# Performance work log

Hardware: AMD Instinct MI355X
Metric: run time of the kernel (lower is better)

The kernel has to match this reference:

```python
import jax, jax.numpy as jnp
import numpy as np

B = 1024          # graphs (games)
NPG = 12          # nodes per hand (to_dense_batch max_num_nodes=12)
N = B * NPG       # nodes per node type
EPG = 72          # edges per graph per edge type
E = B * EPG
CARD = 32         # card embedding dim
HID = 256         # hidden_dim
H = 4             # attention heads
L = 3             # num_layers
FIN = 128         # final_dim
LRELU_SLOPE = float(FIN)  # faithful to nn.LeakyReLU(final_dim) bug


def _make_edges(key):
    k1, k2 = jax.random.split(key)
    g = jnp.repeat(jnp.arange(B, dtype=jnp.int32), EPG)
    src = g * NPG + jax.random.randint(k1, (E,), 0, NPG, dtype=jnp.int32)
    dst = g * NPG + jax.random.randint(k2, (E,), 0, NPG, dtype=jnp.int32)
    return jnp.stack([src, dst])


def setup_inputs() -> dict:
    key = jax.random.key(0)
    ks = jax.random.split(key, 24)
    def nrm(k, shape, fan):
        return jax.random.normal(k, shape, jnp.float32) / np.float32(np.sqrt(fan))
    inp = {
        'x_my': jax.random.normal(ks[0], (N, CARD), jnp.float32),
        'x_opp': jax.random.normal(ks[1], (N, CARD), jnp.float32),
        'edge_beats': _make_edges(ks[2]),
        'edge_loses': _make_edges(ks[3]),
        'edge_rev_beats': _make_edges(ks[4]),
        'edge_rev_loses': _make_edges(ks[5]),
        'batch_my': jnp.repeat(jnp.arange(B, dtype=jnp.int32), NPG),
        # input encoder
        'enc_W': nrm(ks[6], (CARD, HID), CARD), 'enc_b': jnp.zeros((HID,), jnp.float32),
        # GATv2 params, axis1 indexes {0: beats(my->opp), 1: rev_loses_to(opp->my)}
        'gat_Wl': nrm(ks[7], (L, 2, HID, H * HID), HID),
        'gat_bl': jnp.zeros((L, 2, H * HID), jnp.float32),
        'gat_Wr': nrm(ks[8], (L, 2, HID, H * HID), HID),
        'gat_br': jnp.zeros((L, 2, H * HID), jnp.float32),
        'gat_att': nrm(ks[9], (L, 2, H, HID), HID),
        'gat_bias': jnp.zeros((L, 2, HID), jnp.float32),
        # CGConv params, axis1 indexes {0: loses_to(my->opp), 1: rev_beats(opp->my)}
        'cg_Wf': nrm(ks[10], (L, 2, 2 * HID, HID), 2 * HID),
        'cg_bf': jnp.zeros((L, 2, HID), jnp.float32),
        'cg_Ws': nrm(ks[11], (L, 2, 2 * HID, HID), 2 * HID),
        'cg_bs': jnp.zeros((L, 2, HID), jnp.float32),
        # nodewise linear per layer
        'node_W': nrm(ks[12], (L, HID, HID), HID),
        'node_b': jnp.zeros((L, HID), jnp.float32),
        # final encoder
        'fin_W1': nrm(ks[13], (HID, FIN), HID), 'fin_b1': jnp.zeros((FIN,), jnp.float32),
        'fin_W2': nrm(ks[14], (FIN, 1), FIN), 'fin_b2': jnp.zeros((1,), jnp.float32),
    }
    return inp


def _gatv2(x_src, x_dst, edge, Wl, bl, Wr, br, att, bias):
    # PyG GATv2Conv, concat=False, add_self_loops=False, negative_slope=0.2
    Nd = x_dst.shape[0]
    xl = (x_src @ Wl + bl).reshape(-1, H, HID)   # [Ns,H,C]
    xr = (x_dst @ Wr + br).reshape(-1, H, HID)   # [Nd,H,C]
    src, dst = edge[0], edge[1]
    e = jax.nn.leaky_relu(xl[src] + xr[dst], 0.2)            # [E,H,C]
    alpha = jnp.einsum('ehc,hc->eh', e, att)                 # [E,H]
    m = jax.ops.segment_max(alpha, dst, num_segments=Nd)     # softmax by dst
    a = jnp.exp(alpha - m[dst])
    denom = jax.ops.segment_sum(a, dst, num_segments=Nd)
    a = a / (denom[dst] + 1e-16)
    out = jax.ops.segment_sum(a[:, :, None] * xl[src], dst, num_segments=Nd)
    return out.mean(axis=1) + bias                           # mean over heads


def _cgconv(x_src, x_dst, edge, Wf, bf, Ws, bs):
    # PyG CGConv: z = [x_i(dst), x_j(src)]; sigmoid gate * softplus; sum; residual
    src, dst = edge[0], edge[1]
    z = jnp.concatenate([x_dst[dst], x_src[src]], axis=-1)   # [E,2*HID]
    msg = jax.nn.sigmoid(z @ Wf + bf) * jax.nn.softplus(z @ Ws + bs)
    return x_dst + jax.ops.segment_sum(msg, dst, num_segments=x_dst.shape[0])


def reference(x_my, x_opp, edge_beats, edge_loses, edge_rev_beats, edge_rev_loses,
              batch_my, enc_W, enc_b, gat_Wl, gat_bl, gat_Wr, gat_br, gat_att,
              gat_bias, cg_Wf, cg_bf, cg_Ws, cg_bs, node_W, node_b,
              fin_W1, fin_b1, fin_W2, fin_b2):
    h_my = x_my @ enc_W + enc_b
    h_opp = x_opp @ enc_W + enc_b
    for l in range(L):
        # destination opponent_hand: GAT(beats) + CG(loses_to)  (HeteroConv aggr='sum')
        opp_new = _gatv2(h_my, h_opp, edge_beats, gat_Wl[l, 0], gat_bl[l, 0],
                         gat_Wr[l, 0], gat_br[l, 0], gat_att[l, 0], gat_bias[l, 0]) \
                + _cgconv(h_my, h_opp, edge_loses, cg_Wf[l, 0], cg_bf[l, 0],
                          cg_Ws[l, 0], cg_bs[l, 0])
        # destination my_hand: CG(rev_beats) + GAT(rev_loses_to)
        my_new = _cgconv(h_opp, h_my, edge_rev_beats, cg_Wf[l, 1], cg_bf[l, 1],
                         cg_Ws[l, 1], cg_bs[l, 1]) \
               + _gatv2(h_opp, h_my, edge_rev_loses, gat_Wl[l, 1], gat_bl[l, 1],
                        gat_Wr[l, 1], gat_br[l, 1], gat_att[l, 1], gat_bias[l, 1])
        h_my = my_new @ node_W[l] + node_b[l]
        h_opp = opp_new @ node_W[l] + node_b[l]
    f = jax.nn.leaky_relu(h_my @ fin_W1 + fin_b1, LRELU_SLOPE)
    logits = f @ fin_W2 + fin_b2                              # [N,1]
    # to_dense_batch with exactly NPG sorted nodes per graph == reshape
    return logits.reshape(B, NPG)
```

## Files before the change

### kernel.cpp

```cpp
#include <hip/hip_runtime.h>

#define NNODES 12288
#define ETOT   73728
#define NGR    1024
#define LOG2E  1.442695041f
#define LN2    0.6931471806f

typedef __attribute__((ext_vector_type(8))) short short8;
typedef __attribute__((ext_vector_type(4))) float f32x4;

__device__ __forceinline__ unsigned short f2b(float f) {
  return __builtin_bit_cast(unsigned short, (__bf16)f);
}
__device__ __forceinline__ float b2f(unsigned short u) {
  return __uint_as_float(((unsigned)u) << 16);
}
__device__ __forceinline__ void load_lds16(const void* g, void* l) {
  __builtin_amdgcn_global_load_lds(
      (const __attribute__((address_space(1))) unsigned int*)g,
      (__attribute__((address_space(3))) unsigned int*)l, 16, 0, 0);
}
__device__ __forceinline__ unsigned fenc(float f) {
  unsigned u = __float_as_uint(f);
  return (u & 0x80000000u) ? ~u : (u | 0x80000000u);
}
__device__ __forceinline__ float fdec(unsigned e) {
  unsigned u = (e & 0x80000000u) ? (e & 0x7FFFFFFFu) : ~e;
  return __uint_as_float(u);
}

__device__ __forceinline__ const unsigned short* pnode(
    const unsigned short* P, int col0, int node) {
  return P + ((size_t)(col0 >> 7) * NNODES + node) * 128 + (col0 & 127);
}

__global__ void pack_kernel(
    const float* __restrict__ gat_Wl, const float* __restrict__ gat_Wr,
    const float* __restrict__ cg_Wf, const float* __restrict__ cg_Ws,
    const float* __restrict__ node_W, const float* __restrict__ enc_W,
    const float* __restrict__ fin_W1,
    const float* __restrict__ gat_bl, const float* __restrict__ gat_br,
    const float* __restrict__ cg_bf, const float* __restrict__ cg_bs,
    const float* __restrict__ x_my, const float* __restrict__ x_opp,
    unsigned short* __restrict__ wt_my, unsigned short* __restrict__ wt_opp,
    unsigned short* __restrict__ node_wt, unsigned short* __restrict__ enc_wt,
    unsigned short* __restrict__ fin_w1t,
    float* __restrict__ bias_my, float* __restrict__ bias_opp,
    unsigned short* __restrict__ xb)
{
  int idx = blockIdx.x * 256 + threadIdx.x;
  if (idx < 2 * 2359296) {
    int which = idx >= 2359296;
    int t = which ? idx - 2359296 : idx;
    int l = t / 786432;
    int r = t - l * 786432;
    int j = r & 7, lane = (r >> 3) & 63, blk = r >> 9;
    int kb = blk & 7, nb = blk >> 3;
    int n = nb * 16 + (lane & 15);
    int k = kb * 32 + (lane >> 4) * 8 + j;
    float v;
    if (!which) {
      if (n < 1024)      v = gat_Wl[((l*2+0)*256 + k)*1024 + n];
      else if (n < 2048) v = gat_Wr[((l*2+1)*256 + k)*1024 + (n-1024)];
      else if (n < 2304) v = cg_Wf[((l*2+0)*512 + 256 + k)*256 + (n-2048)];
      else if (n < 2560) v = cg_Ws[((l*2+0)*512 + 256 + k)*256 + (n-2304)];
      else if (n < 2816) v = cg_Wf[((l*2+1)*512 + k)*256 + (n-2560)];
      else               v = cg_Ws[((l*2+1)*512 + k)*256 + (n-2816)];
      wt_my[t] = f2b(v);
    } else {
      if (n < 1024)      v = gat_Wr[((l*2+0)*256 + k)*1024 + n];
      else if (n < 2048) v = gat_Wl[((l*2+1)*256 + k)*1024 + (n-1024)];
      else if (n < 2304) v = cg_Wf[((l*2+0)*512 + k)*256 + (n-2048)];
      else if (n < 2560) v = cg_Ws[((l*2+0)*512 + k)*256 + (n-2304)];
      else if (n < 2816) v = cg_Wf[((l*2+1)*512 + 256 + k)*256 + (n-2560)];
      else               v = cg_Ws[((l*2+1)*512 + 256 + k)*256 + (n-2816)];
      wt_opp[t] = f2b(v);
    }
    return;
  }
  idx -= 2 * 2359296;
  if (idx < 196608) {
    int l = idx / 65536, r = idx - l * 65536;
    int j = r & 7, lane = (r >> 3) & 63, blk = r >> 9;
    int kb = blk & 7, nb = blk >> 3;
    int n = nb * 16 + (lane & 15);
    int k = kb * 32 + (lane >> 4) * 8 + j;
    node_wt[idx] = f2b(node_W[(l*256 + k)*256 + n]);
    return;
  }
  idx -= 196608;
  if (idx < 8192) {
    int r = idx;
    int j = r & 7, lane = (r >> 3) & 63, blk = r >> 9;
    int nb = blk;
    int n = nb * 16 + (lane & 15);
    int k = (lane >> 4) * 8 + j;
    enc_wt[idx] = f2b(enc_W[k*256 + n]);
    return;
  }
  idx -= 8192;
  if (idx < 32768) {
    int r = idx;
    int j = r & 7, lane = (r >> 3) & 63, blk = r >> 9;
    int kb = blk & 7, nb = blk >> 3;
    int n = nb * 16 + (lane & 15);
    int k = kb * 32 + (lane >> 4) * 8 + j;
    fin_w1t[idx] = f2b(fin_W1[k*128 + n]);
    return;
  }
  idx -= 32768;
  if (idx < 9216) {
    int l = idx / 3072, n = idx - l * 3072;
    float v;
    if (n < 1024)      v = gat_bl[(l*2+0)*1024 + n];
    else if (n < 2048) v = gat_br[(l*2+1)*1024 + (n-1024)];
    else if (n < 2560) v = 0.f;
    else if (n < 2816) v = cg_bf[(l*2+1)*256 + (n-2560)];
    else               v = cg_bs[(l*2+1)*256 + (n-2816)];
    bias_my[idx] = v;
    return;
  }
  idx -= 9216;
  if (idx < 9216) {
    int l = idx / 3072, n = idx - l * 3072;
    float v;
    if (n < 1024)      v = gat_br[(l*2+0)*1024 + n];
    else if (n < 2048) v = gat_bl[(l*2+1)*1024 + (n-1024)];
    else if (n < 2304) v = cg_bf[(l*2+0)*256 + (n-2048)];
    else if (n < 2560) v = cg_bs[(l*2+0)*256 + (n-2304)];
    else               v = 0.f;
    bias_opp[idx] = v;
    return;
  }
  idx -= 9216;
  if (idx < 2 * 393216) {
    xb[idx] = f2b(idx < 393216 ? x_my[idx] : x_opp[idx - 393216]);
  }
}

__global__ __launch_bounds__(256) void gemm64(
    const unsigned short* __restrict__ A, const unsigned short* __restrict__ Ab,
    int lda,
    const unsigned short* __restrict__ Wp, const unsigned short* __restrict__ Wpb,
    const float* __restrict__ bias, const float* __restrict__ biasb,
    unsigned short* __restrict__ C, unsigned short* __restrict__ Cb,
    int ldc, int K, int act, int bx_split, int colblk)
{
  __shared__ __align__(16) unsigned short lA[64 * 256];
  const int tid = threadIdx.x;
  const int lane = tid & 63;
  const int w = tid >> 6;
  const int wr = w >> 1, wc = w & 1;
  const int r0 = lane & 15, kq = lane >> 4;
  const int KT = K >> 5;
  const int gm = (K >> 3) - 1;
  const int rmask = gm > 7 ? 7 : gm;
  const int gsh = __popc((unsigned)gm);

  const unsigned short *Ap, *Wsel;
  const float* bp;
  unsigned short* Cp;
  int tileM;
  if ((int)blockIdx.x < bx_split) {
    Ap = A;  Wsel = Wp;  bp = bias;  Cp = C;  tileM = blockIdx.x * 64;
  } else {
    Ap = Ab; Wsel = Wpb; bp = biasb; Cp = Cb; tileM = (blockIdx.x - bx_split) * 64;
  }
  const int tileN = blockIdx.y * 128;

  for (int rd = 0; rd < KT; ++rd) {
    int idx = rd * 256 + tid;
    int row = idx >> gsh;
    int g = idx & gm;
    load_lds16(Ap + (size_t)(tileM + row) * lda + ((g ^ (row & rmask)) << 3),
               (char*)lA + idx * 16);
  }

  const int nblk0 = (tileN >> 4) + wc * 4;
  const unsigned short* wn0 = Wsel + ((size_t)(nblk0 + 0) * KT * 64 + lane) * 8;
  const unsigned short* wn1 = Wsel + ((size_t)(nblk0 + 1) * KT * 64 + lane) * 8;
  const unsigned short* wn2 = Wsel + ((size_t)(nblk0 + 2) * KT * 64 + lane) * 8;
  const unsigned short* wn3 = Wsel + ((size_t)(nblk0 + 3) * KT * 64 + lane) * 8;

  short8 b0_0 = *(const short8*)wn0;
  short8 b0_1 = *(const short8*)wn1;
  short8 b0_2 = *(const short8*)wn2;
  short8 b0_3 = *(const short8*)wn3;
  short8 b1_0 = b0_0, b1_1 = b0_1, b1_2 = b0_2, b1_3 = b0_3;
  if (KT > 1) {
    b1_0 = *(const short8*)(wn0 + 512);
    b1_1 = *(const short8*)(wn1 + 512);
    b1_2 = *(const short8*)(wn2 + 512);
    b1_3 = *(const short8*)(wn3 + 512);
  }

  f32x4 acc[2][4];
#pragma unroll
  for (int m = 0; m < 2; ++m)
#pragma unroll
    for (int n = 0; n < 4; ++n)
      acc[m][n] = (f32x4){0.f, 0.f, 0.f, 0.f};

  const int rb0 = (wr * 32 + r0) * K;
  const int rb1 = (wr * 32 + 16 + r0) * K;
  const int rx = r0 & rmask;

  __syncthreads();

  for (int kt = 0; kt < KT; ++kt) {
    short8 b2_0 = b1_0, b2_1 = b1_1, b2_2 = b1_2, b2_3 = b1_3;
    if (kt + 2 < KT) {
      const int o = (kt + 2) * 512;
      b2_0 = *(const short8*)(wn0 + o);
      b2_1 = *(const short8*)(wn1 + o);
      b2_2 = *(const short8*)(wn2 + o);
      b2_3 = *(const short8*)(wn3 + o);
    }
    const int p = (((kt << 2) + kq) ^ rx) * 8;
    short8 af0 = *(const short8*)&lA[rb0 + p];
    short8 af1 = *(const short8*)&lA[rb1 + p];
    acc[0][0] = __builtin_amdgcn_mfma_f32_16x16x32_bf16(b0_0, af0, acc[0][0], 0, 0, 0);
    acc[0][1] = __builtin_amdgcn_mfma_f32_16x16x32_bf16(b0_1, af0, acc[0][1], 0, 0, 0);
    acc[0][2] = __builtin_amdgcn_mfma_f32_16x16x32_bf16(b0_2, af0, acc[0][2], 0, 0, 0);
    acc[0][3] = __builtin_amdgcn_mfma_f32_16x16x32_bf16(b0_3, af0, acc[0][3], 0, 0, 0);
    acc[1][0] = __builtin_amdgcn_mfma_f32_16x16x32_bf16(b0_0, af1, acc[1][0], 0, 0, 0);
    acc[1][1] = __builtin_amdgcn_mfma_f32_16x16x32_bf16(b0_1, af1, acc[1][1], 0, 0, 0);
    acc[1][2] = __builtin_amdgcn_mfma_f32_16x16x32_bf16(b0_2, af1, acc[1][2], 0, 0, 0);
    acc[1][3] = __builtin_amdgcn_mfma_f32_16x16x32_bf16(b0_3, af1, acc[1][3], 0, 0, 0);
    b0_0 = b1_0; b0_1 = b1_1; b0_2 = b1_2; b0_3 = b1_3;
    b1_0 = b2_0; b1_1 = b2_1; b1_2 = b2_2; b1_3 = b2_3;
  }

  unsigned short* cT = lA;
  __syncthreads();
#pragma unroll
  for (int m = 0; m < 2; ++m) {
    const int rl = wr * 32 + m * 16 + r0;
#pragma unroll
    for (int n = 0; n < 4; ++n) {
      const int cl = wc * 64 + n * 16 + kq * 4;
      const f32x4 bv = *(const f32x4*)&bp[tileN + cl];
      float v0 = acc[m][n][0] + bv[0];
      float v1 = acc[m][n][1] + bv[1];
      float v2 = acc[m][n][2] + bv[2];
      float v3 = acc[m][n][3] + bv[3];
      if (act) {
        v0 = v0 > 0.f ? v0 : 128.f * v0;
        v1 = v1 > 0.f ? v1 : 128.f * v1;
        v2 = v2 > 0.f ? v2 : 128.f * v2;
        v3 = v3 > 0.f ? v3 : 128.f * v3;
      }
      uint2 pk;
      pk.x = (unsigned)f2b(v0) | ((unsigned)f2b(v1) << 16);
      pk.y = (unsigned)f2b(v2) | ((unsigned)f2b(v3) << 16);
      *(uint2*)&cT[rl * 132 + cl] = pk;
    }
  }
  __syncthreads();
  if (colblk) {
    unsigned short* dstb = Cp + ((size_t)blockIdx.y * NNODES + tileM) * 128;
#pragma unroll
    for (int it = 0; it < 4; ++it) {
      const int idx = it * 256 + tid;
      const uint4 val = *(const uint4*)&cT[(idx >> 4) * 132 + (idx & 15) * 8];
      *(uint4*)(dstb + (size_t)idx * 8) = val;
    }
  } else {
#pragma unroll
    for (int it = 0; it < 4; ++it) {
      const int idx = it * 256 + tid;
      const int row = idx >> 4, ch = idx & 15;
      const uint4 val = *(const uint4*)&cT[row * 132 + ch * 8];
      *(uint4*)(Cp + (size_t)(tileM + row) * ldc + tileN + ch * 8) = val;
    }
  }
}

#define SX 260
__global__ __launch_bounds__(256) void gat_edge(
    const unsigned short* __restrict__ proj_my,
    const unsigned short* __restrict__ proj_op,
    const int* __restrict__ e_beats, const int* __restrict__ e_rl,
    const float* __restrict__ attL, const float* __restrict__ gbiasL,
    unsigned short* __restrict__ gat_op, unsigned short* __restrict__ gat_my)
{
  __shared__ __align__(16) unsigned short xl[48 * SX];
  __shared__ __align__(16) float attS[4 * SX];
  __shared__ float alphaU[288];
  __shared__ float wU[288];
  __shared__ unsigned mU[48];
  __shared__ float denS[48];
  __shared__ __align__(16) float A2f[12 * 48];
  __shared__ int pmap[144], multI[144], uniqP[144], nuniqS;
  __shared__ unsigned char se8[72], de8[72];
  const int bid = blockIdx.x, tid = threadIdx.x;
  const int dir = bid >= NGR;
  const int g = dir ? bid - NGR : bid;
  const int base = g * 12;

  const unsigned short *Psrc, *Pdst;
  int pcol0;
  const int* edges;
  const float* att;
  const float* gbias;
  unsigned short* outp;
  if (!dir) {
    Psrc = proj_my; Pdst = proj_op; pcol0 = 0;
    edges = e_beats; att = attL; gbias = gbiasL; outp = gat_op;
  } else {
    Psrc = proj_op; Pdst = proj_my; pcol0 = 1024;
    edges = e_rl; att = attL + 1024; gbias = gbiasL + 256; outp = gat_my;
  }

  if (tid < 72) {
    se8[tid] = (unsigned char)(edges[g * 72 + tid] - base);
    de8[tid] = (unsigned char)(edges[ETOT + g * 72 + tid] - base);
  }
  if (tid < 144) { pmap[tid] = -1; multI[tid] = 0; }
  if (tid == 0) nuniqS = 0;
  if (tid < 48) { mU[tid] = 0u; denS[tid] = 0.f; }
  for (int i = tid; i < 576; i += 256) A2f[i] = 0.f;
  for (int i = tid; i < 1024; i += 256)
    attS[(i >> 8) * SX + (i & 255)] = att[i];
  for (int i = tid; i < 3072; i += 256) {
    int s = i >> 8, c4 = (i & 255) * 4;
    int h = c4 >> 8, cc = c4 & 255;
    *(ushort4*)&xl[(h * 12 + s) * SX + cc] =
        *(const ushort4*)pnode(Psrc, pcol0 + c4, base + s);
  }
  __syncthreads();

  if (tid < 72) {
    const int p = (int)de8[tid] * 12 + (int)se8[tid];
    atomicAdd(&multI[p], 1);
    if (atomicCAS(&pmap[p], -1, 0) == -1) {
      const int u = atomicAdd(&nuniqS, 1);
      uniqP[u] = p;
    }
  }
  __syncthreads();
  const int NU4 = nuniqS * 4;

  for (int t = tid; t < NU4; t += 256) {
    const int u = t >> 2, h = t & 3;
    const int p = uniqP[u];
    const int d = p / 12, s = p - d * 12;
    const unsigned short* prA = pnode(Pdst, pcol0 + h * 256, base + d);
    float sum = 0.f;
#pragma unroll
    for (int half = 0; half < 2; ++half) {
      const unsigned short* pr = prA + (size_t)half * (NNODES * 128);
      const unsigned short* pl = &xl[(h * 12 + s) * SX + half * 128];
      const f32x4* pa = (const f32x4*)&attS[h * SX + half * 128];
      for (int q = 0; q < 32; ++q) {
        ushort4 a4 = *(const ushort4*)(pl + q * 4);
        ushort4 b4 = *(const ushort4*)(pr + q * 4);
        f32x4 av = pa[q];
        float v0 = b2f(a4.x) + b2f(b4.x); v0 = fmaxf(v0, 0.2f * v0);
        float v1 = b2f(a4.y) + b2f(b4.y); v1 = fmaxf(v1, 0.2f * v1);
        float v2 = b2f(a4.z) + b2f(b4.z); v2 = fmaxf(v2, 0.2f * v2);
        float v3 = b2f(a4.w) + b2f(b4.w); v3 = fmaxf(v3, 0.2f * v3);
        sum = fmaf(v0, av.x, sum); sum = fmaf(v1, av.y, sum);
        sum = fmaf(v2, av.z, sum); sum = fmaf(v3, av.w, sum);
      }
    }
    sum *= LOG2E;
    alphaU[t] = sum;
    atomicMax(&mU[d * 4 + h], fenc(sum));
  }
  __syncthreads();

  for (int t = tid; t < NU4; t += 256) {
    const int u = t >> 2, h = t & 3;
    const int p = uniqP[u];
    const int d = p / 12;
    const float m = fdec(mU[d * 4 + h]);
    const float wv = __builtin_amdgcn_exp2f(alphaU[t] - m);
    wU[t] = wv;
    atomicAdd(&denS[d * 4 + h], (float)multI[p] * wv);
  }
  __syncthreads();

  for (int t = tid; t < NU4; t += 256) {
    const int u = t >> 2, h = t & 3;
    const int p = uniqP[u];
    const int d = p / 12, s = p - d * 12;
    const float inv = 0.25f * __builtin_amdgcn_rcpf(denS[d * 4 + h] + 1e-16f);
    A2f[d * 48 + h * 12 + s] = (float)multI[p] * wU[t] * inv;
  }
  __syncthreads();

  {
    const int c = tid;
    float xlv[48];
#pragma unroll
    for (int j = 0; j < 48; ++j) xlv[j] = b2f(xl[j * SX + c]);
    const float gb = gbias[c];
#pragma unroll
    for (int d = 0; d < 12; ++d) {
      const f32x4* arow = (const f32x4*)&A2f[d * 48];
      float s = 0.f;
#pragma unroll
      for (int jj = 0; jj < 12; ++jj) {
        f32x4 a4 = arow[jj];
        s = fmaf(a4.x, xlv[jj * 4 + 0], s);
        s = fmaf(a4.y, xlv[jj * 4 + 1], s);
        s = fmaf(a4.z, xlv[jj * 4 + 2], s);
        s = fmaf(a4.w, xlv[jj * 4 + 3], s);
      }
      outp[(size_t)(base + d) * 256 + c] = f2b(s + gb);
    }
  }
}

__global__ __launch_bounds__(256) void cg_edge(
    const unsigned short* __restrict__ proj_my,
    const unsigned short* __restrict__ proj_op,
    const unsigned short* __restrict__ Hmy, const unsigned short* __restrict__ Hopp,
    const unsigned short* __restrict__ gat_my, const unsigned short* __restrict__ gat_op,
    const int* __restrict__ e_loses, const int* __restrict__ e_rb,
    unsigned short* __restrict__ ni_my, unsigned short* __restrict__ ni_op)
{
  __shared__ __align__(8) unsigned short df[3072], dsb[3072];
  __shared__ __align__(8) unsigned short sfb[3072], ssb[3072];
  __shared__ unsigned char srcl[12 * 80];
  __shared__ int cnt[12];
  __shared__ int se_[72], de_[72];
  const int bid = blockIdx.x, tid = threadIdx.x;
  const int dir = bid >= NGR;
  const int g = dir ? bid - NGR : bid;
  const int base = g * 12;

  const unsigned short *Pd, *Ps, *hres, *gatp;
  int fcol, scol;
  const int* edges;
  unsigned short* outp;
  if (!dir) {
    Pd = proj_op; Ps = proj_my; fcol = 2048; scol = 2304;
    hres = Hopp; gatp = gat_op; edges = e_loses; outp = ni_op;
  } else {
    Pd = proj_my; Ps = proj_op; fcol = 2560; scol = 2816;
    hres = Hmy; gatp = gat_my; edges = e_rb; outp = ni_my;
  }

  if (tid < 72) {
    se_[tid] = edges[g * 72 + tid] - base;
    de_[tid] = edges[ETOT + g * 72 + tid] - base;
  }
  for (int i = tid; i < 768; i += 256) {
    int s = i >> 6, c4 = (i & 63) * 4;
    const int node = base + s;
    *(ushort4*)&df[s * 256 + c4]  = *(const ushort4*)pnode(Pd, fcol + c4, node);
    *(ushort4*)&dsb[s * 256 + c4] = *(const ushort4*)pnode(Pd, scol + c4, node);
    *(ushort4*)&sfb[s * 256 + c4] = *(const ushort4*)pnode(Ps, fcol + c4, node);
    *(ushort4*)&ssb[s * 256 + c4] = *(const ushort4*)pnode(Ps, scol + c4, node);
  }
  const int c = tid;
  float hv[12], gv[12];
#pragma unroll
  for (int d = 0; d < 12; ++d) {
    const size_t o = (size_t)(base + d) * 256 + c;
    hv[d] = b2f(hres[o]);
    gv[d] = b2f(gatp[o]);
  }
  __syncthreads();
  if (tid < 12) {
    int n = 0;
    for (int e = 0; e < 72; ++e)
      if (de_[e] == tid) srcl[tid * 80 + (n++)] = (unsigned char)se_[e];
    cnt[tid] = n;
  }
  __syncthreads();
  for (int d = 0; d < 12; ++d) {
    const float fd = b2f(df[d * 256 + c]);
    const float sd = b2f(dsb[d * 256 + c]);
    const int n = cnt[d];
    float acc = 0.f;
    for (int j = 0; j < n; ++j) {
      const int s = srcl[d * 80 + j];
      const float zf = fd + b2f(sfb[s * 256 + c]);
      const float zs = sd + b2f(ssb[s * 256 + c]);
      const float gate = __builtin_amdgcn_rcpf(1.f + __builtin_amdgcn_exp2f(-LOG2E * zf));
      const float e2 = __builtin_amdgcn_exp2f(-LOG2E * fabsf(zs));
      const float sp = fmaxf(zs, 0.f) + LN2 * __builtin_amdgcn_logf(1.f + e2);
      acc = fmaf(gate, sp, acc);
    }
    outp[(size_t)(base + d) * 256 + c] = f2b(hv[d] + gv[d] + acc);
  }
}

__global__ __launch_bounds__(256) void logits_kernel(
    const unsigned short* __restrict__ f, const float* __restrict__ W2,
    const float* __restrict__ b2, float* __restrict__ out)
{
  const int node = blockIdx.x * 4 + (threadIdx.x >> 6);
  const int lane = threadIdx.x & 63;
  const size_t o = (size_t)node * 128 + lane * 2;
  float s = b2f(f[o]) * W2[lane * 2] + b2f(f[o + 1]) * W2[lane * 2 + 1];
  for (int d = 32; d > 0; d >>= 1) s += __shfl_down(s, d, 64);
  if (lane == 0) out[node] = s + b2[0];
}

extern "C" void kernel_launch(void* const* d_in, const int* in_sizes, int n_in,
                              void* d_out, int out_size, void* d_ws, size_t ws_size,
                              hipStream_t stream) {
  const float* x_my    = (const float*)d_in[0];
  const float* x_opp   = (const float*)d_in[1];
  const int*   e_beats = (const int*)d_in[2];
  const int*   e_loses = (const int*)d_in[3];
  const int*   e_rb    = (const int*)d_in[4];
  const int*   e_rl    = (const int*)d_in[5];
  const float* enc_W   = (const float*)d_in[7];
  const float* enc_b   = (const float*)d_in[8];
  const float* gat_Wl  = (const float*)d_in[9];
  const float* gat_bl  = (const float*)d_in[10];
  const float* gat_Wr  = (const float*)d_in[11];
  const float* gat_br  = (const float*)d_in[12];
  const float* gat_att = (const float*)d_in[13];
  const float* gat_bsp = (const float*)d_in[14];
  const float* cg_Wf   = (const float*)d_in[15];
  const float* cg_bf   = (const float*)d_in[16];
  const float* cg_Ws   = (const float*)d_in[17];
  const float* cg_bs   = (const float*)d_in[18];
  const float* node_W  = (const float*)d_in[19];
  const float* node_b  = (const float*)d_in[20];
  const float* fin_W1  = (const float*)d_in[21];
  const float* fin_b1  = (const float*)d_in[22];
  const float* fin_W2  = (const float*)d_in[23];
  const float* fin_b2  = (const float*)d_in[24];

  char* wsp = (char*)d_ws;
  size_t off = 0;
  auto alloc = [&](size_t b) { char* p = wsp + off; off += (b + 255) & ~(size_t)255; return p; };
  unsigned short* wt_my   = (unsigned short*)alloc((size_t)2359296 * 2);
  unsigned short* wt_opp  = (unsigned short*)alloc((size_t)2359296 * 2);
  unsigned short* node_wt = (unsigned short*)alloc((size_t)196608 * 2);
  unsigned short* enc_wt  = (unsigned short*)alloc((size_t)8192 * 2);
  unsigned short* fin_w1t = (unsigned short*)alloc((size_t)32768 * 2);
  float*          bias_my = (float*)alloc((size_t)9216 * 4);
  float*          bias_op = (float*)alloc((size_t)9216 * 4);
  unsigned short* xb      = (unsigned short*)alloc((size_t)786432 * 2);
  unsigned short* Hb      = (unsigned short*)alloc((size_t)2 * NNODES * 256 * 2);
  unsigned short* proj_my = (unsigned short*)alloc((size_t)NNODES * 3072 * 2);
  unsigned short* proj_op = (unsigned short*)alloc((size_t)NNODES * 3072 * 2);
  unsigned short* gat_my  = (unsigned short*)alloc((size_t)NNODES * 256 * 2);
  unsigned short* gat_op  = (unsigned short*)alloc((size_t)NNODES * 256 * 2);
  unsigned short* node_in = (unsigned short*)alloc((size_t)2 * NNODES * 256 * 2);
  unsigned short* fbuf    = (unsigned short*)alloc((size_t)NNODES * 128 * 2);

  const int PACK_TOTAL = 2 * 2359296 + 196608 + 8192 + 32768 + 2 * 9216 + 2 * 393216;
  pack_kernel<<<(PACK_TOTAL + 255) / 256, 256, 0, stream>>>(
      gat_Wl, gat_Wr, cg_Wf, cg_Ws, node_W, enc_W, fin_W1,
      gat_bl, gat_br, cg_bf, cg_bs, x_my, x_opp,
      wt_my, wt_opp, node_wt, enc_wt, fin_w1t, bias_my, bias_op, xb);

  unsigned short* Hmy   = Hb;
  unsigned short* Hopp  = Hb + (size_t)NNODES * 256;
  unsigned short* ni_my = node_in;
  unsigned short* ni_op = node_in + (size_t)NNODES * 256;

  gemm64<<<dim3(384, 2), 256, 0, stream>>>(
      xb, xb, 32, enc_wt, enc_wt, enc_b, enc_b, Hb, Hb, 256, 32, 0, 384, 0);

  for (int l = 0; l < 3; ++l) {
    gemm64<<<dim3(384, 24), 256, 0, stream>>>(
        Hmy, Hopp, 256,
        wt_my + (size_t)l * 786432, wt_opp + (size_t)l * 786432,
        bias_my + l * 3072, bias_op + l * 3072,
        proj_my, proj_op, 3072, 256, 0, 192, 1);
    gat_edge<<<2 * NGR, 256, 0, stream>>>(
        proj_my, proj_op, e_beats, e_rl,
        gat_att + l * 2048, gat_bsp + l * 512, gat_op, gat_my);
    cg_edge<<<2 * NGR, 256, 0, stream>>>(
        proj_my, proj_op, Hmy, Hopp, gat_my, gat_op,
        e_loses, e_rb, ni_my, ni_op);
    gemm64<<<dim3(384, 2), 256, 0, stream>>>(
        node_in, node_in, 256, node_wt + (size_t)l * 65536, node_wt + (size_t)l * 65536,
        node_b + l * 256, node_b + l * 256, Hb, Hb, 256, 256, 0, 384, 0);
  }

  gemm64<<<dim3(192, 1), 256, 0, stream>>>(
      Hmy, Hmy, 256, fin_w1t, fin_w1t, fin_b1, fin_b1, fbuf, fbuf, 128, 256, 1, 192, 0);
  logits_kernel<<<NNODES / 4, 256, 0, stream>>>(fbuf, fin_W2, fin_b2, (float*)d_out);
}
```

Before: 555.5 us.

## Reuse LDS-resident A tile across 12 column blocks in projection GEMM

Adds a specialized projection GEMM kernel that loads the 64x256 A tile into LDS once and loops over 12 output column blocks, instead of launching 24 y-blocks that each reload A. The grid shrinks from 384x24 to 384x2 blocks, and B fragments are register double-buffered two k-steps ahead. This cuts redundant A loads and block launch overhead, but lowers parallelism per launch and serializes work within each block, so there is less latency hiding.

```diff
diff --git a/kernel.cpp b/kernel.cpp
--- a/kernel.cpp
+++ b/kernel.cpp
@@ -144,7 +144,7 @@
     const unsigned short* __restrict__ Wp, const unsigned short* __restrict__ Wpb,
     const float* __restrict__ bias, const float* __restrict__ biasb,
     unsigned short* __restrict__ C, unsigned short* __restrict__ Cb,
-    int ldc, int K, int act, int bx_split, int colblk)
+    int ldc, int K, int act, int bx_split)
 {
   __shared__ __align__(16) unsigned short lA[64 * 256];
   const int tid = threadIdx.x;
@@ -257,21 +257,127 @@
     }
   }
   __syncthreads();
-  if (colblk) {
-    unsigned short* dstb = Cp + ((size_t)blockIdx.y * NNODES + tileM) * 128;
+#pragma unroll
+  for (int it = 0; it < 4; ++it) {
+    const int idx = it * 256 + tid;
+    const int row = idx >> 4, ch = idx & 15;
+    const uint4 val = *(const uint4*)&cT[row * 132 + ch * 8];
+    *(uint4*)(Cp + (size_t)(tileM + row) * ldc + tileN + ch * 8) = val;
+  }
+}
+
+__global__ __launch_bounds__(256) void gemm64p(
+    const unsigned short* __restrict__ A, const unsigned short* __restrict__ Ab,
+    const unsigned short* __restrict__ Wp, const unsigned short* __restrict__ Wpb,
+    const float* __restrict__ bias, const float* __restrict__ biasb,
+    unsigned short* __restrict__ C, unsigned short* __restrict__ Cb,
+    int bx_split)
+{
+  const int K = 256, KT = 8;
+  __shared__ __align__(16) unsigned short lA[64 * 256];
+  __shared__ __align__(16) unsigned short cT[64 * 132];
+  const int tid = threadIdx.x;
+  const int lane = tid & 63;
+  const int w = tid >> 6;
+  const int wr = w >> 1, wc = w & 1;
+  const int r0 = lane & 15, kq = lane >> 4;
+
+  const unsigned short *Ap, *Wsel;
+  const float* bp;
+  unsigned short* Cp;
+  int tileM;
+  if ((int)blockIdx.x < bx_split) {
+    Ap = A;  Wsel = Wp;  bp = bias;  Cp = C;  tileM = blockIdx.x * 64;
+  } else {
+    Ap = Ab; Wsel = Wpb; bp = biasb; Cp = Cb; tileM = (blockIdx.x - bx_split) * 64;
+  }
+
+  for (int rd = 0; rd < KT; ++rd) {
+    int idx = rd * 256 + tid;
+    int row = idx >> 5;
+    int g = idx & 31;
+    load_lds16(Ap + (size_t)(tileM + row) * K + ((g ^ (row & 7)) << 3),
+               (char*)lA + idx * 16);
+  }
+
+  const int rb0 = (wr * 32 + r0) * K;
+  const int rb1 = (wr * 32 + 16 + r0) * K;
+  const int rx = r0 & 7;
+
+  __syncthreads();
+
+  for (int nn = 0; nn < 12; ++nn) {
+    const int cb = (int)blockIdx.y * 12 + nn;
+    const int tileN = cb * 128;
+    const int nblk0 = (tileN >> 4) + wc * 4;
+    const unsigned short* wn0 = Wsel + ((size_t)(nblk0 + 0) * KT * 64 + lane) * 8;
+    const unsigned short* wn1 = Wsel + ((size_t)(nblk0 + 1) * KT * 64 + lane) * 8;
+    const unsigned short* wn2 = Wsel + ((size_t)(nblk0 + 2) * KT * 64 + lane) * 8;
+    const unsigned short* wn3 = Wsel + ((size_t)(nblk0 + 3) * KT * 64 + lane) * 8;
+
+    short8 b0_0 = *(const short8*)wn0;
+    short8 b0_1 = *(const short8*)wn1;
+    short8 b0_2 = *(const short8*)wn2;
+    short8 b0_3 = *(const short8*)wn3;
+    short8 b1_0 = *(const short8*)(wn0 + 512);
+    short8 b1_1 = *(const short8*)(wn1 + 512);
+    short8 b1_2 = *(const short8*)(wn2 + 512);
+    short8 b1_3 = *(const short8*)(wn3 + 512);
+
+    f32x4 acc[2][4];
+#pragma unroll
+    for (int m = 0; m < 2; ++m)
+#pragma unroll
+      for (int n = 0; n < 4; ++n)
+        acc[m][n] = (f32x4){0.f, 0.f, 0.f, 0.f};
+
+    for (int kt = 0; kt < KT; ++kt) {
+      short8 b2_0 = b1_0, b2_1 = b1_1, b2_2 = b1_2, b2_3 = b1_3;
+      if (kt + 2 < KT) {
+        const int o = (kt + 2) * 512;
+        b2_0 = *(const short8*)(wn0 + o);
+        b2_1 = *(const short8*)(wn1 + o);
+        b2_2 = *(const short8*)(wn2 + o);
+        b2_3 = *(const short8*)(wn3 + o);
+      }
+      const int p = (((kt << 2) + kq) ^ rx) * 8;
+      short8 af0 = *(const short8*)&lA[rb0 + p];
+      short8 af1 = *(const short8*)&lA[rb1 + p];
+      acc[0][0] = __builtin_amdgcn_mfma_f32_16x16x32_bf16(b0_0, af0, acc[0][0], 0, 0, 0);
+      acc[0][1] = __builtin_amdgcn_mfma_f32_16x16x32_bf16(b0_1, af0, acc[0][1], 0, 0, 0);
+      acc[0][2] = __builtin_amdgcn_mfma_f32_16x16x32_bf16(b0_2, af0, acc[0][2], 0, 0, 0);
+      acc[0][3] = __builtin_amdgcn_mfma_f32_16x16x32_bf16(b0_3, af0, acc[0][3], 0, 0, 0);
+      acc[1][0] = __builtin_amdgcn_mfma_f32_16x16x32_bf16(b0_0, af1, acc[1][0], 0, 0, 0);
+      acc[1][1] = __builtin_amdgcn_mfma_f32_16x16x32_bf16(b0_1, af1, acc[1][1], 0, 0, 0);
+      acc[1][2] = __builtin_amdgcn_mfma_f32_16x16x32_bf16(b0_2, af1, acc[1][2], 0, 0, 0);
+      acc[1][3] = __builtin_amdgcn_mfma_f32_16x16x32_bf16(b0_3, af1, acc[1][3], 0, 0, 0);
+      b0_0 = b1_0; b0_1 = b1_1; b0_2 = b1_2; b0_3 = b1_3;
+      b1_0 = b2_0; b1_1 = b2_1; b1_2 = b2_2; b1_3 = b2_3;
+    }
+
+    __syncthreads();
+#pragma unroll
+    for (int m = 0; m < 2; ++m) {
+      const int rl = wr * 32 + m * 16 + r0;
+#pragma unroll
+      for (int n = 0; n < 4; ++n) {
+        const int cl = wc * 64 + n * 16 + kq * 4;
+        const f32x4 bv = *(const f32x4*)&bp[tileN + cl];
+        uint2 pk;
+        pk.x = (unsigned)f2b(acc[m][n][0] + bv[0]) |
+               ((unsigned)f2b(acc[m][n][1] + bv[1]) << 16);
+        pk.y = (unsigned)f2b(acc[m][n][2] + bv[2]) |
+               ((unsigned)f2b(acc[m][n][3] + bv[3]) << 16);
+        *(uint2*)&cT[rl * 132 + cl] = pk;
+      }
+    }
+    __syncthreads();
+    unsigned short* dstb = Cp + ((size_t)cb * NNODES + tileM) * 128;
 #pragma unroll
     for (int it = 0; it < 4; ++it) {
       const int idx = it * 256 + tid;
       const uint4 val = *(const uint4*)&cT[(idx >> 4) * 132 + (idx & 15) * 8];
       *(uint4*)(dstb + (size_t)idx * 8) = val;
-    }
-  } else {
-#pragma unroll
-    for (int it = 0; it < 4; ++it) {
-      const int idx = it * 256 + tid;
-      const int row = idx >> 4, ch = idx & 15;
-      const uint4 val = *(const uint4*)&cT[row * 132 + ch * 8];
-      *(uint4*)(Cp + (size_t)(tileM + row) * ldc + tileN + ch * 8) = val;
     }
   }
 }
@@ -560,14 +666,14 @@
   unsigned short* ni_op = node_in + (size_t)NNODES * 256;
 
   gemm64<<<dim3(384, 2), 256, 0, stream>>>(
-      xb, xb, 32, enc_wt, enc_wt, enc_b, enc_b, Hb, Hb, 256, 32, 0, 384, 0);
+      xb, xb, 32, enc_wt, enc_wt, enc_b, enc_b, Hb, Hb, 256, 32, 0, 384);
 
   for (int l = 0; l < 3; ++l) {
-    gemm64<<<dim3(384, 24), 256, 0, stream>>>(
-        Hmy, Hopp, 256,
+    gemm64p<<<dim3(384, 2), 256, 0, stream>>>(
+        Hmy, Hopp,
         wt_my + (size_t)l * 786432, wt_opp + (size_t)l * 786432,
         bias_my + l * 3072, bias_op + l * 3072,
-        proj_my, proj_op, 3072, 256, 0, 192, 1);
+        proj_my, proj_op, 192);
     gat_edge<<<2 * NGR, 256, 0, stream>>>(
         proj_my, proj_op, e_beats, e_rl,
         gat_att + l * 2048, gat_bsp + l * 512, gat_op, gat_my);
@@ -576,10 +682,10 @@
         e_loses, e_rb, ni_my, ni_op);
     gemm64<<<dim3(384, 2), 256, 0, stream>>>(
         node_in, node_in, 256, node_wt + (size_t)l * 65536, node_wt + (size_t)l * 65536,
-        node_b + l * 256, node_b + l * 256, Hb, Hb, 256, 256, 0, 384, 0);
+        node_b + l * 256, node_b + l * 256, Hb, Hb, 256, 256, 0, 384);
   }
 
   gemm64<<<dim3(192, 1), 256, 0, stream>>>(
-      Hmy, Hmy, 256, fin_w1t, fin_w1t, fin_b1, fin_b1, fbuf, fbuf, 128, 256, 1, 192, 0);
+      Hmy, Hmy, 256, fin_w1t, fin_w1t, fin_b1, fin_b1, fbuf, fbuf, 128, 256, 1, 192);
   logits_kernel<<<NNODES / 4, 256, 0, stream>>>(fbuf, fin_W2, fin_b2, (float*)d_out);
 }
```

New measurement: 520.9 us. -6.2%, faster.
